# Kernel tuning notes

Measured on AMD Instinct MI355X. Metric: run time of the kernel, lower is better.

Reference implementation:

```python
import jax, jax.numpy as jnp
import numpy as np

B, L, H_IN, H_RED, H_MLP = 2, 1024, 768, 128, 256

def setup_inputs() -> dict:
    key = jax.random.key(0)
    ks = jax.random.split(key, 7)
    s_in = 1.0 / np.sqrt(H_IN)
    s_p = 1.0 / np.sqrt(2 * H_RED)
    s_m = 1.0 / np.sqrt(H_MLP)
    return {
        "inputs": jax.random.normal(ks[0], (B, L, H_IN), dtype=jnp.float32),
        "Wr": jax.random.uniform(ks[1], (H_RED, H_IN), jnp.float32, -s_in, s_in),
        "br": jax.random.uniform(ks[2], (H_RED,), jnp.float32, -s_in, s_in),
        "W1": jax.random.uniform(ks[3], (H_MLP, 2 * H_RED), jnp.float32, -s_p, s_p),
        "b1": jax.random.uniform(ks[4], (H_MLP,), jnp.float32, -s_p, s_p),
        "W2": jax.random.uniform(ks[5], (1, H_MLP), jnp.float32, -s_m, s_m),
        "b2": jax.random.uniform(ks[6], (1,), jnp.float32, -s_m, s_m),
    }

def reference(inputs, Wr, br, W1, b1, W2, b2):
    # pre_reduction: [B,L,H_IN] -> [B,L,H_RED]
    e = jnp.einsum("blh,rh->blr", inputs, Wr) + br
    b_, l_, r_ = e.shape
    # pairwise concat: row i gets e[i], col j gets e[j] -> [B,L,L,2R]
    row = jnp.broadcast_to(e[:, :, None, :], (b_, l_, l_, r_))
    col = jnp.broadcast_to(e[:, None, :, :], (b_, l_, l_, r_))
    pair = jnp.concatenate([row, col], axis=-1)
    # Lin2D: Linear(2R,256) -> ReLU -> Linear(256,1)
    h = jax.nn.relu(jnp.einsum("bijc,mc->bijm", pair, W1) + b1)
    out = jnp.einsum("bijm,om->bijo", h, W2) + b2  # [B,L,L,1]
    out = out[..., 0]  # [B,L,L]
    # symmetrize: triu(out) + triu(out,1)^T
    upper = jnp.triu(out)
    lower = jnp.swapaxes(jnp.triu(out, k=1), -1, -2)
    return upper + lower
```

## Files before the change

### kernel.cpp

```cpp
#include <hip/hip_runtime.h>

typedef __attribute__((ext_vector_type(4))) float f32x4;
typedef __attribute__((ext_vector_type(8))) short bf16x8;

__device__ inline unsigned short f2bf(float x) {
  unsigned u = __builtin_bit_cast(unsigned, x);
  u += 0x7fffu + ((u >> 16) & 1u);
  return (unsigned short)(u >> 16);
}

__device__ inline bf16x8 pack8(f32x4 lo, f32x4 hi) {
  bf16x8 r;
  r[0] = (short)f2bf(lo[0]); r[1] = (short)f2bf(lo[1]);
  r[2] = (short)f2bf(lo[2]); r[3] = (short)f2bf(lo[3]);
  r[4] = (short)f2bf(hi[0]); r[5] = (short)f2bf(hi[1]);
  r[6] = (short)f2bf(hi[2]); r[7] = (short)f2bf(hi[3]);
  return r;
}

__device__ inline bf16x8 cvt8(const float* __restrict__ p) {
  return pack8(*(const f32x4*)p, *(const f32x4*)(p + 4));
}

__global__ __launch_bounds__(256) void gemm1_kernel(
    const float* __restrict__ X, const float* __restrict__ Wr,
    const float* __restrict__ br, unsigned short* __restrict__ Ebf,
    float* __restrict__ cvec) {
  if (blockIdx.y == 0) {
    int idx = blockIdx.x * 256 + threadIdx.x;
    if (idx < 4096) cvec[idx] = 0.f;
  }
  int wave = threadIdx.x >> 6, lane = threadIdx.x & 63;
  int tok0 = (blockIdx.x * 4 + wave) * 16;
  int n0 = blockIdx.y * 16;
  int lr = lane & 15, kg = (lane >> 4) * 8;
  const float* ap = X + (size_t)(tok0 + lr) * 768 + kg;
  const float* bp = Wr + (size_t)(n0 + lr) * 768 + kg;
  f32x4 acc = {0, 0, 0, 0};
#pragma unroll 4
  for (int k0 = 0; k0 < 768; k0 += 32) {
    bf16x8 a = cvt8(ap + k0);
    bf16x8 b = cvt8(bp + k0);
    acc = __builtin_amdgcn_mfma_f32_16x16x32_bf16(a, b, acc, 0, 0, 0);
  }
  int rb = (lane >> 4) * 4;
  float bias = br[n0 + lr];
#pragma unroll
  for (int r = 0; r < 4; ++r)
    Ebf[(size_t)(tok0 + rb + r) * 128 + n0 + lr] = f2bf(acc[r] + bias);
}

__global__ __launch_bounds__(256) void gemm2_kernel(
    const unsigned short* __restrict__ Ebf, const float* __restrict__ W1,
    const float* __restrict__ b1, const float* __restrict__ W2,
    float* __restrict__ UVt, float* __restrict__ cvec) {
  int wave = threadIdx.x >> 6, lane = threadIdx.x & 63;
  int t0 = blockIdx.x * 64;
  int m0 = (blockIdx.y * 4 + wave) * 16;
  int lr = lane & 15, kg = (lane >> 4) * 8;
  const float* aB = (m0 < 256)
      ? (W1 + (size_t)(m0 + lr) * 256 + kg)
      : (W1 + (size_t)(m0 - 256 + lr) * 256 + 128 + kg);
  f32x4 acc[4] = {{0,0,0,0},{0,0,0,0},{0,0,0,0},{0,0,0,0}};
#pragma unroll
  for (int k0 = 0; k0 < 128; k0 += 32) {
    bf16x8 a = cvt8(aB + k0);
#pragma unroll
    for (int t = 0; t < 4; ++t) {
      bf16x8 b = *(const bf16x8*)(Ebf + (size_t)(t0 + t * 16 + lr) * 128 + kg + k0);
      acc[t] = __builtin_amdgcn_mfma_f32_16x16x32_bf16(a, b, acc[t], 0, 0, 0);
    }
  }
  int rb = (lane >> 4) * 4;
  float p[4] = {0.f, 0.f, 0.f, 0.f};
#pragma unroll
  for (int t = 0; t < 4; ++t) {
#pragma unroll
    for (int r = 0; r < 4; ++r) {
      int m = m0 + rb + r;
      float val = acc[t][r] + ((m0 < 256) ? b1[m] : 0.f);
      UVt[(size_t)m * 2048 + t0 + t * 16 + lr] = val;
      p[t] = fmaf(W2[m & 255], val, p[t]);
    }
  }
#pragma unroll
  for (int t = 0; t < 4; ++t) {
    p[t] += __shfl_xor(p[t], 16);
    p[t] += __shfl_xor(p[t], 32);
  }
  if (lane < 16) {
    int h = (m0 < 256) ? 0 : 1;
#pragma unroll
    for (int t = 0; t < 4; ++t)
      atomicAdd(&cvec[h * 2048 + t0 + t * 16 + lane], 0.5f * p[t]);
  }
}

__global__ __launch_bounds__(256, 2) void pairwise_kernel(
    const float* __restrict__ UVt, const float* __restrict__ W2,
    const float* __restrict__ cvec, const float* __restrict__ b2p,
    float* __restrict__ Out) {
  __shared__ float u_s[4][64][36];
  __shared__ float v_s[4][64][36];
  __shared__ float w2_s[256];
  __shared__ float cuv[64];

  int tid = threadIdx.x;
  int wave = tid >> 6, lane = tid & 63;
  int b = blockIdx.y;
  int p = blockIdx.x;
  int it = 0;
  while (p >= 32 - it) { p -= 32 - it; ++it; }
  int jt = it + p;

  int utok = b * 1024 + it * 32;
  int vtok = b * 1024 + jt * 32;

  w2_s[tid] = W2[tid];
  if (tid < 32) cuv[tid] = cvec[utok + tid];
  else if (tid < 64) cuv[tid] = cvec[2048 + vtok + (tid - 32)];
  __syncthreads();

  int mr = lane >> 3, tq = (lane & 7) * 4;
  int tx = lane & 7, ty = lane >> 3;
  float acc[4][4] = {{0,0,0,0},{0,0,0,0},{0,0,0,0},{0,0,0,0}};

#pragma unroll
  for (int g = 0; g < 8; ++g) {
    int ml = g * 8 + mr;
    int m = wave * 64 + ml;
    *(f32x4*)&u_s[wave][ml][tq] = *(const f32x4*)(UVt + (size_t)m * 2048 + utok + tq);
    *(f32x4*)&v_s[wave][ml][tq] = *(const f32x4*)(UVt + (size_t)(256 + m) * 2048 + vtok + tq);
  }

  for (int ml = 0; ml < 64; ml += 4) {
    f32x4 wq = *(const f32x4*)&w2_s[wave * 64 + ml];
#pragma unroll
    for (int s = 0; s < 4; ++s) {
      f32x4 uu = *(const f32x4*)&u_s[wave][ml + s][4 * ty];
      f32x4 vv = *(const f32x4*)&v_s[wave][ml + s][4 * tx];
      float w = wq[s];
#pragma unroll
      for (int i = 0; i < 4; ++i)
#pragma unroll
        for (int j = 0; j < 4; ++j)
          acc[i][j] = fmaf(w, fabsf(uu[i] + vv[j]), acc[i][j]);
    }
  }

  float* ovp = (float*)u_s;
  float* t2p = (float*)v_s;
  __syncthreads();
#pragma unroll
  for (int i = 0; i < 4; ++i) {
    f32x4 rv = {acc[i][0], acc[i][1], acc[i][2], acc[i][3]};
    *(f32x4*)&ovp[((size_t)wave * 32 + 4 * ty + i) * 36 + 4 * tx] = rv;
  }
  __syncthreads();

  int ly = lane >> 3, tc = lane & 7;
  int row = wave * 8 + ly;
  float b2v = b2p[0];
  f32x4 sum = {0, 0, 0, 0};
#pragma unroll
  for (int q = 0; q < 4; ++q) {
    f32x4 part = *(const f32x4*)&ovp[((size_t)q * 32 + row) * 36 + 4 * tc];
#pragma unroll
    for (int j = 0; j < 4; ++j) sum[j] += part[j];
  }
  float cu = cuv[row];
  f32x4 val;
#pragma unroll
  for (int j = 0; j < 4; ++j)
    val[j] = 0.5f * sum[j] + cu + cuv[32 + 4 * tc + j] + b2v;

  *(f32x4*)&t2p[(size_t)row * 36 + 4 * tc] = val;

  size_t obase = (size_t)b << 20;
  int i0 = it * 32, j0 = jt * 32;
  if (it != jt)
    *(f32x4*)(Out + obase + (size_t)(i0 + row) * 1024 + j0 + 4 * tc) = val;
  else {
#pragma unroll
    for (int j = 0; j < 4; ++j) {
      int jl = 4 * tc + j;
      if (jl >= row) Out[obase + (size_t)(i0 + row) * 1024 + j0 + jl] = val[j];
    }
  }
  __syncthreads();
  f32x4 mv;
#pragma unroll
  for (int j = 0; j < 4; ++j) mv[j] = t2p[(size_t)(4 * tc + j) * 36 + row];
  if (it != jt)
    *(f32x4*)(Out + obase + (size_t)(j0 + row) * 1024 + i0 + 4 * tc) = mv;
  else {
#pragma unroll
    for (int j = 0; j < 4; ++j) {
      int c = 4 * tc + j;
      if (row > c) Out[obase + (size_t)(i0 + row) * 1024 + j0 + c] = mv[j];
    }
  }
}

extern "C" void kernel_launch(void* const* d_in, const int* in_sizes, int n_in,
                              void* d_out, int out_size, void* d_ws, size_t ws_size,
                              hipStream_t stream) {
  (void)in_sizes; (void)n_in; (void)out_size; (void)ws_size;
  const float* X  = (const float*)d_in[0];
  const float* Wr = (const float*)d_in[1];
  const float* br = (const float*)d_in[2];
  const float* W1 = (const float*)d_in[3];
  const float* b1 = (const float*)d_in[4];
  const float* W2 = (const float*)d_in[5];
  const float* b2 = (const float*)d_in[6];
  float* Out = (float*)d_out;

  char* ws = (char*)d_ws;
  unsigned short* Ebf  = (unsigned short*)(ws);
  float*          UVt  = (float*)(ws + 524288);
  float*          cvec = (float*)(ws + 4718592);

  gemm1_kernel<<<dim3(32, 8), 256, 0, stream>>>(X, Wr, br, Ebf, cvec);
  gemm2_kernel<<<dim3(32, 8), 256, 0, stream>>>(Ebf, W1, b1, W2, UVt, cvec);
  pairwise_kernel<<<dim3(528, 2), 256, 0, stream>>>(UVt, W2, cvec, b2, Out);
}
```

Measured before the change: 55.69 us.

## Fuse three kernels into one persistent kernel with grid barriers

Replaces the two GEMM kernels and the pairwise kernel with a single persistent kernel of 256 blocks that runs each stage in turn, separated by software grid-wide barriers built on atomics, and loops over the pairwise tiles. This is meant to remove the launch gaps between kernels. In exchange it adds a memset for the barrier counters, spin-wait barriers that assume all 256 blocks are resident at once, and a pairwise stage that now runs at fixed residency instead of using the 1056-block launch.

```diff
diff --git a/kernel.cpp b/kernel.cpp
--- a/kernel.cpp
+++ b/kernel.cpp
@@ -22,182 +22,203 @@
   return pack8(*(const f32x4*)p, *(const f32x4*)(p + 4));
 }
 
-__global__ __launch_bounds__(256) void gemm1_kernel(
+__device__ __forceinline__ void grid_barrier(unsigned* bar, unsigned nblk) {
+  __syncthreads();
+  if (threadIdx.x == 0) {
+    __threadfence();
+    unsigned gen = __hip_atomic_load(bar + 1, __ATOMIC_RELAXED,
+                                     __HIP_MEMORY_SCOPE_AGENT);
+    unsigned arrived = __hip_atomic_fetch_add(bar, 1u, __ATOMIC_ACQ_REL,
+                                              __HIP_MEMORY_SCOPE_AGENT);
+    if (arrived == nblk - 1u) {
+      __hip_atomic_store(bar, 0u, __ATOMIC_RELAXED, __HIP_MEMORY_SCOPE_AGENT);
+      __hip_atomic_fetch_add(bar + 1, 1u, __ATOMIC_RELEASE,
+                             __HIP_MEMORY_SCOPE_AGENT);
+    } else {
+      int t = 0;
+      while (__hip_atomic_load(bar + 1, __ATOMIC_ACQUIRE,
+                               __HIP_MEMORY_SCOPE_AGENT) == gen) {
+        __builtin_amdgcn_s_sleep(8);
+        if (++t > (1 << 20)) break;
+      }
+    }
+    __threadfence();
+  }
+  __syncthreads();
+}
+
+__global__ __launch_bounds__(256) void mega_kernel(
     const float* __restrict__ X, const float* __restrict__ Wr,
-    const float* __restrict__ br, unsigned short* __restrict__ Ebf,
-    float* __restrict__ cvec) {
-  if (blockIdx.y == 0) {
-    int idx = blockIdx.x * 256 + threadIdx.x;
-    if (idx < 4096) cvec[idx] = 0.f;
-  }
-  int wave = threadIdx.x >> 6, lane = threadIdx.x & 63;
-  int tok0 = (blockIdx.x * 4 + wave) * 16;
-  int n0 = blockIdx.y * 16;
-  int lr = lane & 15, kg = (lane >> 4) * 8;
-  const float* ap = X + (size_t)(tok0 + lr) * 768 + kg;
-  const float* bp = Wr + (size_t)(n0 + lr) * 768 + kg;
-  f32x4 acc = {0, 0, 0, 0};
-#pragma unroll 4
-  for (int k0 = 0; k0 < 768; k0 += 32) {
-    bf16x8 a = cvt8(ap + k0);
-    bf16x8 b = cvt8(bp + k0);
-    acc = __builtin_amdgcn_mfma_f32_16x16x32_bf16(a, b, acc, 0, 0, 0);
-  }
-  int rb = (lane >> 4) * 4;
-  float bias = br[n0 + lr];
-#pragma unroll
-  for (int r = 0; r < 4; ++r)
-    Ebf[(size_t)(tok0 + rb + r) * 128 + n0 + lr] = f2bf(acc[r] + bias);
-}
-
-__global__ __launch_bounds__(256) void gemm2_kernel(
-    const unsigned short* __restrict__ Ebf, const float* __restrict__ W1,
+    const float* __restrict__ br, const float* __restrict__ W1,
     const float* __restrict__ b1, const float* __restrict__ W2,
-    float* __restrict__ UVt, float* __restrict__ cvec) {
-  int wave = threadIdx.x >> 6, lane = threadIdx.x & 63;
-  int t0 = blockIdx.x * 64;
-  int m0 = (blockIdx.y * 4 + wave) * 16;
-  int lr = lane & 15, kg = (lane >> 4) * 8;
-  const float* aB = (m0 < 256)
-      ? (W1 + (size_t)(m0 + lr) * 256 + kg)
-      : (W1 + (size_t)(m0 - 256 + lr) * 256 + 128 + kg);
-  f32x4 acc[4] = {{0,0,0,0},{0,0,0,0},{0,0,0,0},{0,0,0,0}};
-#pragma unroll
-  for (int k0 = 0; k0 < 128; k0 += 32) {
-    bf16x8 a = cvt8(aB + k0);
-#pragma unroll
-    for (int t = 0; t < 4; ++t) {
-      bf16x8 b = *(const bf16x8*)(Ebf + (size_t)(t0 + t * 16 + lr) * 128 + kg + k0);
-      acc[t] = __builtin_amdgcn_mfma_f32_16x16x32_bf16(a, b, acc[t], 0, 0, 0);
-    }
-  }
-  int rb = (lane >> 4) * 4;
-  float p[4] = {0.f, 0.f, 0.f, 0.f};
-#pragma unroll
-  for (int t = 0; t < 4; ++t) {
-#pragma unroll
-    for (int r = 0; r < 4; ++r) {
-      int m = m0 + rb + r;
-      float val = acc[t][r] + ((m0 < 256) ? b1[m] : 0.f);
-      UVt[(size_t)m * 2048 + t0 + t * 16 + lr] = val;
-      p[t] = fmaf(W2[m & 255], val, p[t]);
-    }
-  }
-#pragma unroll
-  for (int t = 0; t < 4; ++t) {
-    p[t] += __shfl_xor(p[t], 16);
-    p[t] += __shfl_xor(p[t], 32);
-  }
-  if (lane < 16) {
-    int h = (m0 < 256) ? 0 : 1;
-#pragma unroll
-    for (int t = 0; t < 4; ++t)
-      atomicAdd(&cvec[h * 2048 + t0 + t * 16 + lane], 0.5f * p[t]);
-  }
-}
-
-__global__ __launch_bounds__(256, 2) void pairwise_kernel(
-    const float* __restrict__ UVt, const float* __restrict__ W2,
-    const float* __restrict__ cvec, const float* __restrict__ b2p,
-    float* __restrict__ Out) {
+    const float* __restrict__ b2p, unsigned short* __restrict__ Ebf,
+    float* __restrict__ UVt, float* __restrict__ cvec,
+    unsigned* __restrict__ bar, float* __restrict__ Out) {
   __shared__ float u_s[4][64][36];
   __shared__ float v_s[4][64][36];
   __shared__ float w2_s[256];
   __shared__ float cuv[64];
 
-  int tid = threadIdx.x;
-  int wave = tid >> 6, lane = tid & 63;
-  int b = blockIdx.y;
-  int p = blockIdx.x;
-  int it = 0;
-  while (p >= 32 - it) { p -= 32 - it; ++it; }
-  int jt = it + p;
-
-  int utok = b * 1024 + it * 32;
-  int vtok = b * 1024 + jt * 32;
-
-  w2_s[tid] = W2[tid];
-  if (tid < 32) cuv[tid] = cvec[utok + tid];
-  else if (tid < 64) cuv[tid] = cvec[2048 + vtok + (tid - 32)];
-  __syncthreads();
-
-  int mr = lane >> 3, tq = (lane & 7) * 4;
-  int tx = lane & 7, ty = lane >> 3;
-  float acc[4][4] = {{0,0,0,0},{0,0,0,0},{0,0,0,0},{0,0,0,0}};
-
-#pragma unroll
-  for (int g = 0; g < 8; ++g) {
-    int ml = g * 8 + mr;
-    int m = wave * 64 + ml;
-    *(f32x4*)&u_s[wave][ml][tq] = *(const f32x4*)(UVt + (size_t)m * 2048 + utok + tq);
-    *(f32x4*)&v_s[wave][ml][tq] = *(const f32x4*)(UVt + (size_t)(256 + m) * 2048 + vtok + tq);
-  }
-
-  for (int ml = 0; ml < 64; ml += 4) {
-    f32x4 wq = *(const f32x4*)&w2_s[wave * 64 + ml];
-#pragma unroll
-    for (int s = 0; s < 4; ++s) {
-      f32x4 uu = *(const f32x4*)&u_s[wave][ml + s][4 * ty];
-      f32x4 vv = *(const f32x4*)&v_s[wave][ml + s][4 * tx];
-      float w = wq[s];
-#pragma unroll
-      for (int i = 0; i < 4; ++i)
-#pragma unroll
-        for (int j = 0; j < 4; ++j)
-          acc[i][j] = fmaf(w, fabsf(uu[i] + vv[j]), acc[i][j]);
-    }
-  }
-
-  float* ovp = (float*)u_s;
-  float* t2p = (float*)v_s;
-  __syncthreads();
-#pragma unroll
-  for (int i = 0; i < 4; ++i) {
-    f32x4 rv = {acc[i][0], acc[i][1], acc[i][2], acc[i][3]};
-    *(f32x4*)&ovp[((size_t)wave * 32 + 4 * ty + i) * 36 + 4 * tx] = rv;
-  }
-  __syncthreads();
-
-  int ly = lane >> 3, tc = lane & 7;
-  int row = wave * 8 + ly;
-  float b2v = b2p[0];
-  f32x4 sum = {0, 0, 0, 0};
-#pragma unroll
-  for (int q = 0; q < 4; ++q) {
-    f32x4 part = *(const f32x4*)&ovp[((size_t)q * 32 + row) * 36 + 4 * tc];
-#pragma unroll
-    for (int j = 0; j < 4; ++j) sum[j] += part[j];
-  }
-  float cu = cuv[row];
-  f32x4 val;
-#pragma unroll
-  for (int j = 0; j < 4; ++j)
-    val[j] = 0.5f * sum[j] + cu + cuv[32 + 4 * tc + j] + b2v;
-
-  *(f32x4*)&t2p[(size_t)row * 36 + 4 * tc] = val;
-
-  size_t obase = (size_t)b << 20;
-  int i0 = it * 32, j0 = jt * 32;
-  if (it != jt)
-    *(f32x4*)(Out + obase + (size_t)(i0 + row) * 1024 + j0 + 4 * tc) = val;
-  else {
-#pragma unroll
-    for (int j = 0; j < 4; ++j) {
-      int jl = 4 * tc + j;
-      if (jl >= row) Out[obase + (size_t)(i0 + row) * 1024 + j0 + jl] = val[j];
-    }
-  }
-  __syncthreads();
-  f32x4 mv;
-#pragma unroll
-  for (int j = 0; j < 4; ++j) mv[j] = t2p[(size_t)(4 * tc + j) * 36 + row];
-  if (it != jt)
-    *(f32x4*)(Out + obase + (size_t)(j0 + row) * 1024 + i0 + 4 * tc) = mv;
-  else {
-#pragma unroll
-    for (int j = 0; j < 4; ++j) {
-      int c = 4 * tc + j;
-      if (row > c) Out[obase + (size_t)(i0 + row) * 1024 + j0 + c] = mv[j];
+  int tid = threadIdx.x, wave = tid >> 6, lane = tid & 63;
+  int lr = lane & 15, kg = (lane >> 4) * 8;
+  int rb = (lane >> 4) * 4;
+
+  if (tid < 16) cvec[blockIdx.x * 16 + tid] = 0.f;
+  {
+    int w = blockIdx.x * 4 + wave;
+    int tok0 = (w >> 3) * 16, n0 = (w & 7) * 16;
+    const float* ap = X + (size_t)(tok0 + lr) * 768 + kg;
+    const float* bp = Wr + (size_t)(n0 + lr) * 768 + kg;
+    f32x4 acc = {0, 0, 0, 0};
+#pragma unroll 4
+    for (int k0 = 0; k0 < 768; k0 += 32) {
+      bf16x8 a = cvt8(ap + k0);
+      bf16x8 b = cvt8(bp + k0);
+      acc = __builtin_amdgcn_mfma_f32_16x16x32_bf16(a, b, acc, 0, 0, 0);
+    }
+    float bias = br[n0 + lr];
+#pragma unroll
+    for (int r = 0; r < 4; ++r)
+      Ebf[(size_t)(tok0 + rb + r) * 128 + n0 + lr] = f2bf(acc[r] + bias);
+  }
+  grid_barrier(bar, 256);
+
+  {
+    int w = blockIdx.x * 4 + wave;
+    int t0 = (w >> 5) * 64;
+    int m0 = (w & 31) * 16;
+    const float* aB = (m0 < 256)
+        ? (W1 + (size_t)(m0 + lr) * 256 + kg)
+        : (W1 + (size_t)(m0 - 256 + lr) * 256 + 128 + kg);
+    f32x4 acc[4] = {{0,0,0,0},{0,0,0,0},{0,0,0,0},{0,0,0,0}};
+#pragma unroll
+    for (int k0 = 0; k0 < 128; k0 += 32) {
+      bf16x8 a = cvt8(aB + k0);
+#pragma unroll
+      for (int t = 0; t < 4; ++t) {
+        bf16x8 b = *(const bf16x8*)(Ebf + (size_t)(t0 + t * 16 + lr) * 128 + kg + k0);
+        acc[t] = __builtin_amdgcn_mfma_f32_16x16x32_bf16(a, b, acc[t], 0, 0, 0);
+      }
+    }
+    float p[4] = {0.f, 0.f, 0.f, 0.f};
+#pragma unroll
+    for (int t = 0; t < 4; ++t) {
+#pragma unroll
+      for (int r = 0; r < 4; ++r) {
+        int m = m0 + rb + r;
+        float val = acc[t][r] + ((m0 < 256) ? b1[m] : 0.f);
+        UVt[(size_t)m * 2048 + t0 + t * 16 + lr] = val;
+        p[t] = fmaf(W2[m & 255], val, p[t]);
+      }
+    }
+#pragma unroll
+    for (int t = 0; t < 4; ++t) {
+      p[t] += __shfl_xor(p[t], 16);
+      p[t] += __shfl_xor(p[t], 32);
+    }
+    if (lane < 16) {
+      int h = (m0 < 256) ? 0 : 1;
+#pragma unroll
+      for (int t = 0; t < 4; ++t)
+        atomicAdd(&cvec[h * 2048 + t0 + t * 16 + lane], 0.5f * p[t]);
+    }
+  }
+  grid_barrier(bar + 16, 256);
+
+  for (int task = blockIdx.x; task < 1056; task += 256) {
+    __syncthreads();
+    int b = task >= 528 ? 1 : 0;
+    int p = task - b * 528;
+    int it = 0;
+    while (p >= 32 - it) { p -= 32 - it; ++it; }
+    int jt = it + p;
+
+    int utok = b * 1024 + it * 32;
+    int vtok = b * 1024 + jt * 32;
+
+    w2_s[tid] = W2[tid];
+    if (tid < 32) cuv[tid] = cvec[utok + tid];
+    else if (tid < 64) cuv[tid] = cvec[2048 + vtok + (tid - 32)];
+    __syncthreads();
+
+    int mr = lane >> 3, tq = (lane & 7) * 4;
+    int tx = lane & 7, ty = lane >> 3;
+    float acc[4][4] = {{0,0,0,0},{0,0,0,0},{0,0,0,0},{0,0,0,0}};
+
+#pragma unroll
+    for (int g = 0; g < 8; ++g) {
+      int ml = g * 8 + mr;
+      int m = wave * 64 + ml;
+      *(f32x4*)&u_s[wave][ml][tq] = *(const f32x4*)(UVt + (size_t)m * 2048 + utok + tq);
+      *(f32x4*)&v_s[wave][ml][tq] = *(const f32x4*)(UVt + (size_t)(256 + m) * 2048 + vtok + tq);
+    }
+
+    for (int ml = 0; ml < 64; ml += 4) {
+      f32x4 wq = *(const f32x4*)&w2_s[wave * 64 + ml];
+#pragma unroll
+      for (int s = 0; s < 4; ++s) {
+        f32x4 uu = *(const f32x4*)&u_s[wave][ml + s][4 * ty];
+        f32x4 vv = *(const f32x4*)&v_s[wave][ml + s][4 * tx];
+        float w = wq[s];
+#pragma unroll
+        for (int i = 0; i < 4; ++i)
+#pragma unroll
+          for (int j = 0; j < 4; ++j)
+            acc[i][j] = fmaf(w, fabsf(uu[i] + vv[j]), acc[i][j]);
+      }
+    }
+
+    float* ovp = (float*)u_s;
+    float* t2p = (float*)v_s;
+    __syncthreads();
+#pragma unroll
+    for (int i = 0; i < 4; ++i) {
+      f32x4 rv = {acc[i][0], acc[i][1], acc[i][2], acc[i][3]};
+      *(f32x4*)&ovp[((size_t)wave * 32 + 4 * ty + i) * 36 + 4 * tx] = rv;
+    }
+    __syncthreads();
+
+    int tc = lane & 7;
+    int row = wave * 8 + (lane >> 3);
+    float b2v = b2p[0];
+    f32x4 sum = {0, 0, 0, 0};
+#pragma unroll
+    for (int q = 0; q < 4; ++q) {
+      f32x4 part = *(const f32x4*)&ovp[((size_t)q * 32 + row) * 36 + 4 * tc];
+#pragma unroll
+      for (int j = 0; j < 4; ++j) sum[j] += part[j];
+    }
+    float cu = cuv[row];
+    f32x4 val;
+#pragma unroll
+    for (int j = 0; j < 4; ++j)
+      val[j] = 0.5f * sum[j] + cu + cuv[32 + 4 * tc + j] + b2v;
+
+    *(f32x4*)&t2p[(size_t)row * 36 + 4 * tc] = val;
+
+    size_t obase = (size_t)b << 20;
+    int i0 = it * 32, j0 = jt * 32;
+    if (it != jt)
+      *(f32x4*)(Out + obase + (size_t)(i0 + row) * 1024 + j0 + 4 * tc) = val;
+    else {
+#pragma unroll
+      for (int j = 0; j < 4; ++j) {
+        int jl = 4 * tc + j;
+        if (jl >= row) Out[obase + (size_t)(i0 + row) * 1024 + j0 + jl] = val[j];
+      }
+    }
+    __syncthreads();
+    f32x4 mv;
+#pragma unroll
+    for (int j = 0; j < 4; ++j) mv[j] = t2p[(size_t)(4 * tc + j) * 36 + row];
+    if (it != jt)
+      *(f32x4*)(Out + obase + (size_t)(j0 + row) * 1024 + i0 + 4 * tc) = mv;
+    else {
+#pragma unroll
+      for (int j = 0; j < 4; ++j) {
+        int c = 4 * tc + j;
+        if (row > c) Out[obase + (size_t)(i0 + row) * 1024 + j0 + c] = mv[j];
+      }
     }
   }
 }
@@ -216,11 +237,12 @@
   float* Out = (float*)d_out;
 
   char* ws = (char*)d_ws;
-  unsigned short* Ebf  = (unsigned short*)(ws);
-  float*          UVt  = (float*)(ws + 524288);
-  float*          cvec = (float*)(ws + 4718592);
-
-  gemm1_kernel<<<dim3(32, 8), 256, 0, stream>>>(X, Wr, br, Ebf, cvec);
-  gemm2_kernel<<<dim3(32, 8), 256, 0, stream>>>(Ebf, W1, b1, W2, UVt, cvec);
-  pairwise_kernel<<<dim3(528, 2), 256, 0, stream>>>(UVt, W2, cvec, b2, Out);
-}
+  unsigned*       bar  = (unsigned*)(ws);
+  unsigned short* Ebf  = (unsigned short*)(ws + 128);
+  float*          UVt  = (float*)(ws + 524416);
+  float*          cvec = (float*)(ws + 4718720);
+
+  hipMemsetAsync(bar, 0, 128, stream);
+  mega_kernel<<<256, 256, 0, stream>>>(X, Wr, br, W1, b1, W2, b2, Ebf, UVt,
+                                       cvec, bar, Out);
+}
```

Result: slower. 135.0 us (+142.5%).
